# Kernel tuning notes

Hardware: AMD Instinct MI355X
Metric: run time of the kernel (lower is better)

Reference implementation:

```python
import jax, jax.numpy as jnp
import numpy as np

IN_FEATURES = 1024
OUT_FEATURES = 1024
N = 8192

def setup_inputs() -> dict:
    key = jax.random.key(0)
    kx, kw, kb = jax.random.split(key, 3)
    x = jax.random.normal(kx, (N, IN_FEATURES), dtype=jnp.float32)
    # nn.Linear default init: U(-1/sqrt(in), 1/sqrt(in))
    bound = 1.0 / np.sqrt(IN_FEATURES)
    W = jax.random.uniform(kw, (OUT_FEATURES, IN_FEATURES), minval=-bound, maxval=bound, dtype=jnp.float32)
    b = jax.random.uniform(kb, (OUT_FEATURES,), minval=-bound, maxval=bound, dtype=jnp.float32)
    return {"x": x, "W": W, "b": b}

def reference(x, W, b):
    # h: [N, D]
    h = x @ W.T + b
    # scores: [N, N]; tanh applied to raw scores, softmax over dim=1 (rows)
    scores = jnp.tanh(h @ h.T)
    attn = jax.nn.softmax(scores, axis=1)
    out = jnp.tanh(attn @ h)
    return out
```

## Files before the change

kernel.cpp:

```cpp
#include <hip/hip_runtime.h>
#include <hip/hip_bf16.h>
#include <cstdint>
#include <cstddef>

typedef __bf16 bf16_t;
typedef __bf16 bf16x4 __attribute__((ext_vector_type(4)));
typedef __bf16 bf16x8 __attribute__((ext_vector_type(8)));
typedef float f32x4 __attribute__((ext_vector_type(4)));
typedef float f32x16 __attribute__((ext_vector_type(16)));
typedef float f32x2 __attribute__((ext_vector_type(2)));
typedef int i32x4 __attribute__((ext_vector_type(4)));
typedef int i32x8 __attribute__((ext_vector_type(8)));

#define NROWS 8192
#define DFEAT 1024
#define BK 32
#define NBLK 64
#define TILE_B (128 * BK)
#define F8TILE 8192
#define NB2 32
#define NTRI2 528

typedef __attribute__((address_space(3))) unsigned int lds_uint;
typedef __attribute__((address_space(1))) const unsigned int glb_uint;

__device__ __forceinline__ float fast_tanh(float x) {
  float e = __expf(2.0f * x);
  return 1.0f - 2.0f * __builtin_amdgcn_rcpf(e + 1.0f);
}

__device__ __forceinline__ unsigned pack_fp8x4(float a, float b, float c, float d) {
  unsigned v = 0;
  v = __builtin_amdgcn_cvt_pk_fp8_f32(a, b, v, false);
  v = __builtin_amdgcn_cvt_pk_fp8_f32(c, d, v, true);
  return v;
}

__global__ __launch_bounds__(256) void cast_kernel(const float* __restrict__ in,
                                                   bf16_t* __restrict__ out, int n4) {
  int i = blockIdx.x * 256 + threadIdx.x;
  if (i < n4) {
    float4 v = *(const float4*)(in + i * 4);
    bf16x4 o = {(bf16_t)v.x, (bf16_t)v.y, (bf16_t)v.z, (bf16_t)v.w};
    *(bf16x4*)(out + i * 4) = o;
  }
}

__device__ __forceinline__ void stage_async(const bf16_t* __restrict__ g, int ld,
                                            int row0, int k0, bf16_t* lds,
                                            int wave, int lane) {
#pragma unroll
  for (int t = 0; t < 2; ++t) {
    const int rb = (t * 4 + wave) * 16;
    const bf16_t* gp = g + (size_t)(row0 + rb + (lane >> 2)) * ld + (k0 + (lane & 3) * 8);
    __builtin_amdgcn_global_load_lds((glb_uint*)gp, (lds_uint*)(lds + rb * BK), 16, 0, 0);
  }
}

__device__ __forceinline__ void stage_f8(const uint8_t* __restrict__ g, int ld,
                                         int row0, int k0, uint8_t* lds,
                                         int wave, int lane) {
#pragma unroll
  for (int t = 0; t < 2; ++t) {
    const int rb = (t * 4 + wave) * 16;
    const uint8_t* gp = g + (size_t)(row0 + rb + (lane >> 2)) * ld + (k0 + (lane & 3) * 16);
    __builtin_amdgcn_global_load_lds((glb_uint*)gp, (lds_uint*)(lds + rb * 64), 16, 0, 0);
  }
}

__device__ __forceinline__ void stage256(const bf16_t* __restrict__ g,
                                         int row0, int kt, bf16_t* lds,
                                         int wave, int lane) {
  const int cg = (lane & 7) ^ ((wave * 4 + (lane >> 4)) & 7);
#pragma unroll
  for (int o = 0; o < 4; ++o) {
    const int row = o * 64 + wave * 8 + (lane >> 3);
    const bf16_t* gp = g + (size_t)(row0 + row) * DFEAT + kt * 64 + cg * 8;
    __builtin_amdgcn_global_load_lds((glb_uint*)gp,
        (lds_uint*)(lds + o * 4096 + wave * 512 + lane * 8), 16, 0, 0);
  }
}

__global__ __launch_bounds__(256) void gemm1_kernel(const bf16_t* __restrict__ xb,
                                                    const bf16_t* __restrict__ Wb,
                                                    const float* __restrict__ bias,
                                                    bf16_t* __restrict__ hout,
                                                    uint8_t* __restrict__ hT8) {
  __shared__ __align__(16) bf16_t smem[4 * TILE_B];
  const int tid = threadIdx.x;
  const int wave = tid >> 6, lane = tid & 63;
  const int wm = wave >> 1, wn = wave & 1;
  const int l15 = lane & 15, quad = lane >> 4;
  const int m0 = blockIdx.x * 128, n0 = blockIdx.y * 128;
  f32x4 acc[4][4] = {};
  const int NIT = DFEAT / BK;
  stage_async(xb, DFEAT, m0, 0, smem, wave, lane);
  stage_async(Wb, DFEAT, n0, 0, smem + TILE_B, wave, lane);
  __syncthreads();
  for (int it = 0; it < NIT; ++it) {
    bf16_t* lA = smem + (it & 1) * 2 * TILE_B;
    bf16_t* lB = lA + TILE_B;
    if (it + 1 < NIT) {
      bf16_t* nA = smem + ((it + 1) & 1) * 2 * TILE_B;
      stage_async(xb, DFEAT, m0, (it + 1) * BK, nA, wave, lane);
      stage_async(Wb, DFEAT, n0, (it + 1) * BK, nA + TILE_B, wave, lane);
    }
    bf16x8 a[4], b[4];
#pragma unroll
    for (int f = 0; f < 4; ++f) {
      a[f] = *(const bf16x8*)(lA + (wm * 64 + f * 16 + l15) * BK + quad * 8);
      b[f] = *(const bf16x8*)(lB + (wn * 64 + f * 16 + l15) * BK + quad * 8);
    }
#pragma unroll
    for (int i = 0; i < 4; ++i)
#pragma unroll
      for (int j = 0; j < 4; ++j)
        acc[i][j] = __builtin_amdgcn_mfma_f32_16x16x32_bf16(a[i], b[j], acc[i][j], 0, 0, 0);
    __syncthreads();
  }
#pragma unroll
  for (int i = 0; i < 4; ++i) {
    int rbase = m0 + wm * 64 + i * 16 + quad * 4;
#pragma unroll
    for (int j = 0; j < 4; ++j) {
      int col = n0 + wn * 64 + j * 16 + l15;
      float bv = bias[col];
      float hv[4];
#pragma unroll
      for (int r = 0; r < 4; ++r) hv[r] = acc[i][j][r] + bv;
#pragma unroll
      for (int r = 0; r < 4; ++r)
        hout[(size_t)(rbase + r) * DFEAT + col] = (bf16_t)hv[r];
      *(unsigned*)(hT8 + (size_t)col * NROWS + rbase) =
          pack_fp8x4(hv[0], hv[1], hv[2], hv[3]);
    }
  }
}

__global__ __launch_bounds__(512, 1) void scores_sym_kernel(const bf16_t* __restrict__ h,
                                                            uint8_t* __restrict__ P,
                                                            float* __restrict__ lsum) {
  __shared__ __align__(16) char smem_raw[131072];
  bf16_t* smb = (bf16_t*)smem_raw;
  uint8_t (*mir)[272] = (uint8_t(*)[272])smem_raw;

  const int k = (int)blockIdx.x & 7;
  const int s = (int)blockIdx.x >> 3;
  int I, J, r, c;
  if (s < 10) {
    I = J = k;
    int tt = s; r = 0;
    while (tt >= 4 - r) { tt -= 4 - r; ++r; }
    c = r + tt;
  } else {
    int e, t;
    if (s < 58) { e = 3 * k + (s - 10) / 16; t = (s - 10) & 15; }
    else { e = 24 + (k >> 1); t = ((k & 1) << 3) + (s - 58); }
    int ee = e; I = 0;
    while (ee >= 7 - I) { ee -= 7 - I; ++I; }
    J = I + 1 + ee;
    r = t >> 2; c = t & 3;
  }
  const int bm = I * 4 + r, bn = J * 4 + c;
  const bool offdiag = (bm != bn);
  const int m0 = bm * 256, n0 = bn * 256;

  const int tid = threadIdx.x;
  const int wave = tid >> 6, lane = tid & 63;
  const int wm = wave >> 2, wn = wave & 3;
  const int l15 = lane & 15, quad = lane >> 4;
  const int rkey = (l15 >> 1) & 7;

  f32x4 acc[8][4] = {};
  const int NKT = DFEAT / 64;

  stage256(h, m0, 0, smb, wave, lane);
  stage256(h, n0, 0, smb + 16384, wave, lane);
  __syncthreads();
  for (int kt = 0; kt < NKT; ++kt) {
    bf16_t* bufA = smb + (kt & 1) * 32768;
    bf16_t* bufB = bufA + 16384;
    if (kt + 1 < NKT) {
      bf16_t* nA = smb + ((kt + 1) & 1) * 32768;
      stage256(h, m0, kt + 1, nA, wave, lane);
      stage256(h, n0, kt + 1, nA + 16384, wave, lane);
    }
#pragma unroll
    for (int ks = 0; ks < 2; ++ks) {
      const int cp = ((ks * 4 + quad) ^ rkey) * 8;
      bf16x8 a[8], b[4];
#pragma unroll
      for (int mf = 0; mf < 8; ++mf)
        a[mf] = *(const bf16x8*)(bufA + (wm * 128 + mf * 16 + l15) * 64 + cp);
#pragma unroll
      for (int nf = 0; nf < 4; ++nf)
        b[nf] = *(const bf16x8*)(bufB + (wn * 64 + nf * 16 + l15) * 64 + cp);
#pragma unroll
      for (int mf = 0; mf < 8; ++mf)
#pragma unroll
        for (int nf = 0; nf < 4; ++nf)
          acc[mf][nf] = __builtin_amdgcn_mfma_f32_16x16x32_bf16(a[mf], b[nf], acc[mf][nf], 0, 0, 0);
    }
    __syncthreads();
  }

  float rs[8][4];
  float cs[4];
#pragma unroll
  for (int i = 0; i < 8; ++i)
#pragma unroll
    for (int r2 = 0; r2 < 4; ++r2) rs[i][r2] = 0.f;
#pragma unroll
  for (int j = 0; j < 4; ++j) cs[j] = 0.f;

#pragma unroll
  for (int i = 0; i < 8; ++i) {
    const int rl_loc = wm * 128 + i * 16 + quad * 4;
    const int rbase = m0 + rl_loc;
#pragma unroll
    for (int j = 0; j < 4; ++j) {
      const int cl_loc = wn * 64 + j * 16 + l15;
      const int col = n0 + cl_loc;
      float p[4];
#pragma unroll
      for (int r2 = 0; r2 < 4; ++r2) p[r2] = __expf(fast_tanh(acc[i][j][r2]));
      unsigned packed = pack_fp8x4(p[0], p[1], p[2], p[3]);
      f32x2 d0 = __builtin_amdgcn_cvt_pk_f32_fp8(packed, false);
      f32x2 d1 = __builtin_amdgcn_cvt_pk_f32_fp8(packed, true);
      float q[4] = {d0.x, d0.y, d1.x, d1.y};
#pragma unroll
      for (int r2 = 0; r2 < 4; ++r2) {
        rs[i][r2] += q[r2];
        cs[j] += q[r2];
        P[(size_t)(rbase + r2) * NROWS + col] = (uint8_t)(packed >> (8 * r2));
      }
      if (offdiag) *(unsigned*)&mir[cl_loc][rl_loc] = packed;
    }
  }

#pragma unroll
  for (int off = 1; off < 16; off <<= 1)
#pragma unroll
    for (int i = 0; i < 8; ++i)
#pragma unroll
      for (int r2 = 0; r2 < 4; ++r2) rs[i][r2] += __shfl_xor(rs[i][r2], off, 64);
  if (l15 == 0) {
#pragma unroll
    for (int i = 0; i < 8; ++i) {
      int rbase = m0 + wm * 128 + i * 16 + quad * 4;
#pragma unroll
      for (int r2 = 0; r2 < 4; ++r2) atomicAdd(&lsum[rbase + r2], rs[i][r2]);
    }
  }

  if (offdiag) {
#pragma unroll
    for (int off = 16; off < 64; off <<= 1)
#pragma unroll
      for (int j = 0; j < 4; ++j) cs[j] += __shfl_xor(cs[j], off, 64);
    if (quad == 0) {
#pragma unroll
      for (int j = 0; j < 4; ++j)
        atomicAdd(&lsum[n0 + wn * 64 + j * 16 + l15], cs[j]);
    }
    __syncthreads();
#pragma unroll
    for (int it = 0; it < 8; ++it) {
      int q2 = tid + it * 512;
      int c2 = q2 >> 4, r0 = (q2 & 15) * 16;
      uint4 v = *(const uint4*)(&mir[c2][r0]);
      *(uint4*)(P + (size_t)(n0 + c2) * NROWS + m0 + r0) = v;
    }
  }
}

__global__ __launch_bounds__(256) void pv_kernel(const uint8_t* __restrict__ P,
                                                 const uint8_t* __restrict__ hT8,
                                                 const float* __restrict__ lsum,
                                                 float* __restrict__ out) {
  __shared__ __align__(16) uint8_t smem[4 * F8TILE];
  const int tid = threadIdx.x;
  const int wave = tid >> 6, lane = tid & 63;
  const int wm = wave >> 1, wn = wave & 1;
  const int l31 = lane & 31, khalf = lane >> 5;
  const int m0 = blockIdx.x * 128, n0 = blockIdx.y * 128;
  f32x16 acc[2][2] = {};
  const int NIT = NROWS / 64;
  stage_f8(P, NROWS, m0, 0, smem, wave, lane);
  stage_f8(hT8, NROWS, n0, 0, smem + F8TILE, wave, lane);
  __syncthreads();
  for (int it = 0; it < NIT; ++it) {
    uint8_t* lA = smem + (it & 1) * 2 * F8TILE;
    uint8_t* lB = lA + F8TILE;
    if (it + 1 < NIT) {
      uint8_t* nA = smem + ((it + 1) & 1) * 2 * F8TILE;
      stage_f8(P, NROWS, m0, (it + 1) * 64, nA, wave, lane);
      stage_f8(hT8, NROWS, n0, (it + 1) * 64, nA + F8TILE, wave, lane);
    }
    i32x8 a[2], b[2];
#pragma unroll
    for (int f = 0; f < 2; ++f) {
      {
        int off = (wm * 64 + f * 32 + l31) * 64 + khalf * 32;
        i32x4 lo = *(const i32x4*)(lA + off);
        i32x4 hi = *(const i32x4*)(lA + off + 16);
        a[f] = i32x8{lo[0], lo[1], lo[2], lo[3], hi[0], hi[1], hi[2], hi[3]};
      }
      {
        int off = (wn * 64 + f * 32 + l31) * 64 + khalf * 32;
        i32x4 lo = *(const i32x4*)(lB + off);
        i32x4 hi = *(const i32x4*)(lB + off + 16);
        b[f] = i32x8{lo[0], lo[1], lo[2], lo[3], hi[0], hi[1], hi[2], hi[3]};
      }
    }
#pragma unroll
    for (int bi = 0; bi < 2; ++bi)
#pragma unroll
      for (int bj = 0; bj < 2; ++bj)
        acc[bi][bj] = __builtin_amdgcn_mfma_scale_f32_32x32x64_f8f6f4(
            a[bi], b[bj], acc[bi][bj], 0, 0, 0, 0x7F7F7F7F, 0, 0x7F7F7F7F);
    __syncthreads();
  }
#pragma unroll
  for (int bi = 0; bi < 2; ++bi)
#pragma unroll
    for (int bj = 0; bj < 2; ++bj) {
      int cbase = n0 + wn * 64 + bj * 32 + l31;
#pragma unroll
      for (int reg = 0; reg < 16; ++reg) {
        int row = m0 + wm * 64 + bi * 32 + (reg & 3) + 8 * (reg >> 2) + 4 * khalf;
        float rl = __builtin_amdgcn_rcpf(lsum[row]);
        out[(size_t)row * DFEAT + cbase] = fast_tanh(acc[bi][bj][reg] * rl);
      }
    }
}

extern "C" void kernel_launch(void* const* d_in, const int* in_sizes, int n_in,
                              void* d_out, int out_size, void* d_ws, size_t ws_size,
                              hipStream_t stream) {
  const float* x = (const float*)d_in[0];
  const float* W = (const float*)d_in[1];
  const float* bias = (const float*)d_in[2];
  float* out = (float*)d_out;

  bf16_t* xb = (bf16_t*)d_ws;
  bf16_t* Wb = xb + (size_t)NROWS * DFEAT;
  bf16_t* h  = Wb + (size_t)DFEAT * DFEAT;
  uint8_t* hT8 = (uint8_t*)(h + (size_t)NROWS * DFEAT);
  float* lsum = (float*)(hT8 + (size_t)DFEAT * NROWS);
  uint8_t* P = (uint8_t*)(lsum + NROWS);

  cast_kernel<<<(NROWS * DFEAT / 4) / 256, 256, 0, stream>>>(x, xb, NROWS * DFEAT / 4);
  cast_kernel<<<(DFEAT * DFEAT / 4) / 256, 256, 0, stream>>>(W, Wb, DFEAT * DFEAT / 4);
  gemm1_kernel<<<dim3(NROWS / 128, DFEAT / 128), 256, 0, stream>>>(xb, Wb, bias, h, hT8);
  hipMemsetAsync(lsum, 0, NROWS * sizeof(float), stream);
  scores_sym_kernel<<<NTRI2, 512, 0, stream>>>(h, P, lsum);
  pv_kernel<<<dim3(NROWS / 128, DFEAT / 128), 256, 0, stream>>>(P, hT8, lsum, out);
}
```

Measured before the change: 314.7 us.

## Remap symmetric score tiles per XCD and skip duplicate B staging on diagonals

```diff
diff --git a/kernel.cpp b/kernel.cpp
--- a/kernel.cpp
+++ b/kernel.cpp
@@ -11,6 +11,7 @@
 typedef float f32x2 __attribute__((ext_vector_type(2)));
 typedef int i32x4 __attribute__((ext_vector_type(4)));
 typedef int i32x8 __attribute__((ext_vector_type(8)));
+typedef unsigned int u32x4 __attribute__((ext_vector_type(4)));
 
 #define NROWS 8192
 #define DFEAT 1024
@@ -145,23 +146,22 @@
   uint8_t (*mir)[272] = (uint8_t(*)[272])smem_raw;
 
   const int k = (int)blockIdx.x & 7;
-  const int s = (int)blockIdx.x >> 3;
-  int I, J, r, c;
-  if (s < 10) {
-    I = J = k;
-    int tt = s; r = 0;
-    while (tt >= 4 - r) { tt -= 4 - r; ++r; }
-    c = r + tt;
-  } else {
-    int e, t;
-    if (s < 58) { e = 3 * k + (s - 10) / 16; t = (s - 10) & 15; }
-    else { e = 24 + (k >> 1); t = ((k & 1) << 3) + (s - 58); }
-    int ee = e; I = 0;
-    while (ee >= 7 - I) { ee -= 7 - I; ++I; }
-    J = I + 1 + ee;
-    r = t >> 2; c = t & 3;
-  }
-  const int bm = I * 4 + r, bn = J * 4 + c;
+  int s = (int)blockIdx.x >> 3;
+  int bm, bn;
+  {
+    const int L0 = 31 - k;
+    const int L1 = k;
+    const int L2n = 23 - k;
+    if (s < L0) { bm = k; bn = k + 1 + s; }
+    else if ((s -= L0) < L1) { bm = 31 - k; bn = 32 - k + s; }
+    else if ((s -= L1) < L2n) { bm = k + 8; bn = k + 9 + s; }
+    else if ((s -= L2n) < 8 + k) { bm = 23 - k; bn = 24 - k + s; }
+    else {
+      int d = s - (8 + k);
+      bm = (d == 0) ? k : (d == 1) ? (31 - k) : (d == 2) ? (k + 8) : (23 - k);
+      bn = bm;
+    }
+  }
   const bool offdiag = (bm != bn);
   const int m0 = bm * 256, n0 = bn * 256;
 
@@ -175,15 +175,15 @@
   const int NKT = DFEAT / 64;
 
   stage256(h, m0, 0, smb, wave, lane);
-  stage256(h, n0, 0, smb + 16384, wave, lane);
+  if (offdiag) stage256(h, n0, 0, smb + 16384, wave, lane);
   __syncthreads();
   for (int kt = 0; kt < NKT; ++kt) {
     bf16_t* bufA = smb + (kt & 1) * 32768;
-    bf16_t* bufB = bufA + 16384;
+    bf16_t* bufB = offdiag ? bufA + 16384 : bufA;
     if (kt + 1 < NKT) {
       bf16_t* nA = smb + ((kt + 1) & 1) * 32768;
       stage256(h, m0, kt + 1, nA, wave, lane);
-      stage256(h, n0, kt + 1, nA + 16384, wave, lane);
+      if (offdiag) stage256(h, n0, kt + 1, nA + 16384, wave, lane);
     }
 #pragma unroll
     for (int ks = 0; ks < 2; ++ks) {
@@ -268,8 +268,8 @@
     for (int it = 0; it < 8; ++it) {
       int q2 = tid + it * 512;
       int c2 = q2 >> 4, r0 = (q2 & 15) * 16;
-      uint4 v = *(const uint4*)(&mir[c2][r0]);
-      *(uint4*)(P + (size_t)(n0 + c2) * NROWS + m0 + r0) = v;
+      u32x4 v = *(const u32x4*)(&mir[c2][r0]);
+      *(u32x4*)(P + (size_t)(n0 + c2) * NROWS + m0 + r0) = v;
     }
   }
 }
```

Result: slower. 332.3 us (+5.6%).

## Store P transposed with packed writes and skip duplicate staging on diagonal tiles

Applied to the files above, without the earlier changes.

```diff
diff --git a/kernel.cpp b/kernel.cpp
--- a/kernel.cpp
+++ b/kernel.cpp
@@ -11,6 +11,7 @@
 typedef float f32x2 __attribute__((ext_vector_type(2)));
 typedef int i32x4 __attribute__((ext_vector_type(4)));
 typedef int i32x8 __attribute__((ext_vector_type(8)));
+typedef unsigned int u32x4 __attribute__((ext_vector_type(4)));
 
 #define NROWS 8192
 #define DFEAT 1024
@@ -147,15 +148,15 @@
   const int k = (int)blockIdx.x & 7;
   const int s = (int)blockIdx.x >> 3;
   int I, J, r, c;
-  if (s < 10) {
-    I = J = k;
-    int tt = s; r = 0;
-    while (tt >= 4 - r) { tt -= 4 - r; ++r; }
-    c = r + tt;
+  if (s >= 62) {
+    I = J = k; r = c = s - 62;
+  } else if (s < 6) {
+    const int rr[6] = {0, 0, 0, 1, 1, 2}, cc[6] = {1, 2, 3, 2, 3, 3};
+    I = J = k; r = rr[s]; c = cc[s];
   } else {
     int e, t;
-    if (s < 58) { e = 3 * k + (s - 10) / 16; t = (s - 10) & 15; }
-    else { e = 24 + (k >> 1); t = ((k & 1) << 3) + (s - 58); }
+    if (s < 54) { e = 3 * k + (s - 6) / 16; t = (s - 6) & 15; }
+    else { e = 24 + (k >> 1); t = ((k & 1) << 3) + (s - 54); }
     int ee = e; I = 0;
     while (ee >= 7 - I) { ee -= 7 - I; ++I; }
     J = I + 1 + ee;
@@ -175,15 +176,15 @@
   const int NKT = DFEAT / 64;
 
   stage256(h, m0, 0, smb, wave, lane);
-  stage256(h, n0, 0, smb + 16384, wave, lane);
+  if (offdiag) stage256(h, n0, 0, smb + 16384, wave, lane);
   __syncthreads();
   for (int kt = 0; kt < NKT; ++kt) {
     bf16_t* bufA = smb + (kt & 1) * 32768;
-    bf16_t* bufB = bufA + 16384;
+    bf16_t* bufB = offdiag ? bufA + 16384 : bufA;
     if (kt + 1 < NKT) {
       bf16_t* nA = smb + ((kt + 1) & 1) * 32768;
       stage256(h, m0, kt + 1, nA, wave, lane);
-      stage256(h, n0, kt + 1, nA + 16384, wave, lane);
+      if (offdiag) stage256(h, n0, kt + 1, nA + 16384, wave, lane);
     }
 #pragma unroll
     for (int ks = 0; ks < 2; ++ks) {
@@ -216,11 +217,9 @@
 #pragma unroll
   for (int i = 0; i < 8; ++i) {
     const int rl_loc = wm * 128 + i * 16 + quad * 4;
-    const int rbase = m0 + rl_loc;
 #pragma unroll
     for (int j = 0; j < 4; ++j) {
       const int cl_loc = wn * 64 + j * 16 + l15;
-      const int col = n0 + cl_loc;
       float p[4];
 #pragma unroll
       for (int r2 = 0; r2 < 4; ++r2) p[r2] = __expf(fast_tanh(acc[i][j][r2]));
@@ -232,9 +231,13 @@
       for (int r2 = 0; r2 < 4; ++r2) {
         rs[i][r2] += q[r2];
         cs[j] += q[r2];
-        P[(size_t)(rbase + r2) * NROWS + col] = (uint8_t)(packed >> (8 * r2));
-      }
-      if (offdiag) *(unsigned*)&mir[cl_loc][rl_loc] = packed;
+      }
+      *(unsigned*)(P + (size_t)(n0 + cl_loc) * NROWS + (m0 + rl_loc)) = packed;
+      if (offdiag) {
+#pragma unroll
+        for (int r2 = 0; r2 < 4; ++r2)
+          mir[rl_loc + r2][cl_loc] = (uint8_t)(packed >> (8 * r2));
+      }
     }
   }
 
@@ -267,9 +270,9 @@
 #pragma unroll
     for (int it = 0; it < 8; ++it) {
       int q2 = tid + it * 512;
-      int c2 = q2 >> 4, r0 = (q2 & 15) * 16;
-      uint4 v = *(const uint4*)(&mir[c2][r0]);
-      *(uint4*)(P + (size_t)(n0 + c2) * NROWS + m0 + r0) = v;
+      int row = q2 >> 4, c0 = (q2 & 15) * 16;
+      u32x4 v = *(const u32x4*)(&mir[row][c0]);
+      *(u32x4*)(P + (size_t)(m0 + row) * NROWS + n0 + c0) = v;
     }
   }
 }
```

After: 321.5 us. 1.02x slower.
